# Performance work log

Hardware: AMD Instinct MI355X
Metric: run time of the kernel (lower is better)

Reference implementation:

```python
import jax, jax.numpy as jnp
import numpy as np

B, S, D, H, F = 2, 2048, 1024, 16, 4096
HD = D // H
NEG_INF = jnp.float32(-1e30)


def layer_norm(x, gamma, beta, eps=1e-6):
    mu = jnp.mean(x, axis=-1, keepdims=True)
    var = jnp.mean(jnp.square(x - mu), axis=-1, keepdims=True)
    return (x - mu) * jax.lax.rsqrt(var + eps) * gamma + beta


def setup_inputs() -> dict:
    key = jax.random.key(0)
    ks = jax.random.split(key, 8)
    d = np.sqrt(float(D))
    dx_up = np.sqrt(6.0 / (D + F))
    dx_dn = np.sqrt(6.0 / (F + D))
    return {
        "x_embeds": jax.random.normal(ks[0], (B, S, D), dtype=jnp.float32),
        "tokens": jax.random.randint(ks[1], (B, S), 0, 128, dtype=jnp.int32),
        "KQV": jax.random.uniform(ks[2], (D, 3 * D), jnp.float32, -1 / d, 1 / d),
        "WO": jax.random.uniform(ks[3], (D, D), jnp.float32, -1 / d, 1 / d),
        "W_up": jax.random.uniform(ks[4], (D, F), jnp.float32, -dx_up, dx_up),
        "b_up": jnp.zeros((F,), jnp.float32),
        "W_down": jax.random.uniform(ks[5], (F, D), jnp.float32, -dx_dn, dx_dn),
        "b_down": jnp.zeros((D,), jnp.float32),
        "ln1_g": jnp.ones((D,), jnp.float32),
        "ln1_b": jnp.zeros((D,), jnp.float32),
        "ln2_g": jnp.ones((D,), jnp.float32),
        "ln2_b": jnp.zeros((D,), jnp.float32),
        "start_token_id": 1,
    }


def reference(x_embeds, tokens, KQV, WO, W_up, b_up, W_down, b_down,
              ln1_g, ln1_b, ln2_g, ln2_b, start_token_id):
    b, s = x_embeds.shape[0], x_embeds.shape[1]
    # --- attention ---
    x_kqv = jnp.einsum("bsd,de->bse", x_embeds, KQV)          # [B,S,3D]
    x_kqv = x_kqv.reshape(b, s, H, 3, HD)
    k = x_kqv[:, :, :, 0, :]   # [B,S,H,HD]
    q = x_kqv[:, :, :, 1, :]
    v = x_kqv[:, :, :, 2, :]
    inner = jnp.einsum("bqhd,bkhd->bhqk", q, k)               # [B,H,S,S]
    # causal mask
    causal = jnp.tril(jnp.ones((s, s), dtype=bool))           # [S,S]
    # block-diagonal document mask from start tokens
    seg = jnp.cumsum((tokens == start_token_id).astype(jnp.int32), axis=1)  # [B,S]
    same_seg = seg[:, :, None] == seg[:, None, :]             # [B,S,S]
    mask = causal[None, None] & same_seg[:, None]             # [B,1->H,S,S]
    inner = jnp.where(mask, inner, NEG_INF)
    dk = jnp.sqrt(jnp.float32(HD))
    WA = jax.nn.softmax(inner / dk, axis=-1)
    head_outs = jnp.einsum("bhqk,bkhd->bqhd", WA, v)          # [B,S,H,HD]
    out = head_outs.reshape(b, s, D) @ WO
    out = layer_norm(out, ln1_g, ln1_b)
    x = out + x_embeds
    # --- ffnn ---
    h = jax.nn.relu(x @ W_up + b_up)
    out = h @ W_down + b_down
    out = layer_norm(out, ln2_g, ln2_b)
    return out + x
```

## Files before the change

### kernel.cpp

```cpp
#include <hip/hip_runtime.h>

typedef unsigned short u16;
typedef unsigned int u32;
typedef __bf16 bf16_t;
typedef bf16_t bf16x8 __attribute__((ext_vector_type(8)));
typedef u16 u16x8 __attribute__((ext_vector_type(8)));
typedef float f32x4 __attribute__((ext_vector_type(4)));

__device__ __forceinline__ float bf2f(u16 u) {
    union { float f; unsigned i; } c; c.i = ((unsigned)u) << 16; return c.f;
}
__device__ __forceinline__ u16 f2bf(float f) {
    return __builtin_bit_cast(u16, (bf16_t)f);
}
__device__ __forceinline__ f32x4 mfma16(bf16x8 a, bf16x8 b, f32x4 c) {
    return __builtin_amdgcn_mfma_f32_16x16x32_bf16(a, b, c, 0, 0, 0);
}
__device__ __forceinline__ void gld16(const u16* g, u16* l) {
    __builtin_amdgcn_global_load_lds(
        (const __attribute__((address_space(1))) void*)g,
        (__attribute__((address_space(3))) void*)l, 16, 0, 0);
}

__global__ __launch_bounds__(256)
void cvt_kernel(const float* __restrict__ in, u16* __restrict__ out)
{
    const int i = (blockIdx.x * 256 + threadIdx.x) * 8;
    float4 a = *reinterpret_cast<const float4*>(in + i);
    float4 b = *reinterpret_cast<const float4*>(in + i + 4);
    u16x8 o;
    o[0] = f2bf(a.x); o[1] = f2bf(a.y); o[2] = f2bf(a.z); o[3] = f2bf(a.w);
    o[4] = f2bf(b.x); o[5] = f2bf(b.y); o[6] = f2bf(b.z); o[7] = f2bf(b.w);
    *reinterpret_cast<u16x8*>(out + i) = o;
}

__global__ __launch_bounds__(256)
void cvt_t_kernel(const float* __restrict__ in, u16* __restrict__ out,
                  int K, int N)
{
    __shared__ float tile[32][33];
    const int kb = blockIdx.x * 32, nb = blockIdx.y * 32;
    const int r = threadIdx.x >> 3, c4 = threadIdx.x & 7;
    float4 v = *reinterpret_cast<const float4*>(&in[(size_t)(kb + r) * N + nb + c4 * 4]);
    tile[r][c4 * 4 + 0] = v.x; tile[r][c4 * 4 + 1] = v.y;
    tile[r][c4 * 4 + 2] = v.z; tile[r][c4 * 4 + 3] = v.w;
    __syncthreads();
    ushort4 o;
    o.x = f2bf(tile[c4 * 4 + 0][r]);
    o.y = f2bf(tile[c4 * 4 + 1][r]);
    o.z = f2bf(tile[c4 * 4 + 2][r]);
    o.w = f2bf(tile[c4 * 4 + 3][r]);
    *reinterpret_cast<ushort4*>(&out[(size_t)(nb + r) * K + kb + c4 * 4]) = o;
}

template<int NSPLIT, bool BIAS, bool RELU, bool QSCALE>
__global__ __launch_bounds__(512, 4)
void gemm8w_kernel(const u16* __restrict__ A, const u16* __restrict__ Bt,
                   const float* __restrict__ bias, u16* __restrict__ C,
                   int M, int N, int K)
{
    __shared__ u16 As[128][64];
    __shared__ u16 Bs[128][64];
    const int tid  = threadIdx.x;
    const int lane = tid & 63;
    const int wid  = tid >> 6;
    const int wm = wid >> 2, wn = wid & 3;
    const int bm = blockIdx.x, bn = blockIdx.y;
    const int kg = lane >> 4;
    const int lc = lane & 15;
    const int pk = kg ^ ((lc + (lc >> 2)) & 3);

    f32x4 acc[4][2];
    #pragma unroll
    for (int i = 0; i < 4; ++i)
        #pragma unroll
        for (int j = 0; j < 2; ++j)
            acc[i][j] = f32x4{0.f, 0.f, 0.f, 0.f};

    const int nk = (K >> 6) / NSPLIT;
    const int kbase = (NSPLIT > 1) ? blockIdx.z * nk : 0;

    for (int kt = 0; kt < nk; ++kt) {
        const int ktg = kbase + kt;
        __syncthreads();
        #pragma unroll
        for (int p = 0; p < 2; ++p) {
            int c = p * 512 + tid;
            int row  = c >> 3;
            int half = (c >> 2) & 1;
            int ko   = (((c & 3) ^ ((row + (row >> 2)) & 3)) << 3) + half * 32;
            gld16(A + (size_t)(bm * 128 + row) * K + ktg * 64 + ko,
                  &As[0][0] + c * 8);
            gld16(Bt + (size_t)(bn * 128 + row) * K + ktg * 64 + ko,
                  &Bs[0][0] + c * 8);
        }
        __syncthreads();

        bf16x8 af[4][2], bf[2][2];
        #pragma unroll
        for (int i = 0; i < 4; ++i)
            #pragma unroll
            for (int kk = 0; kk < 2; ++kk)
                af[i][kk] = *reinterpret_cast<const bf16x8*>(
                    &As[wm * 64 + i * 16 + lc][kk * 32 + pk * 8]);
        #pragma unroll
        for (int j = 0; j < 2; ++j)
            #pragma unroll
            for (int kk = 0; kk < 2; ++kk)
                bf[j][kk] = *reinterpret_cast<const bf16x8*>(
                    &Bs[wn * 32 + j * 16 + lc][kk * 32 + pk * 8]);
        #pragma unroll
        for (int j = 0; j < 2; ++j)
            #pragma unroll
            for (int i = 0; i < 4; ++i)
                #pragma unroll
                for (int kk = 0; kk < 2; ++kk)
                    acc[i][j] = mfma16(af[i][kk], bf[j][kk], acc[i][j]);
    }

    u16* Cp = C + (size_t)((NSPLIT > 1) ? blockIdx.z : 0) * M * N;
    const bool addb = BIAS && (NSPLIT == 1 || blockIdx.z == 0);
    #pragma unroll
    for (int i = 0; i < 4; ++i) {
        #pragma unroll
        for (int j = 0; j < 2; ++j) {
            int col = bn * 128 + wn * 32 + j * 16 + lc;
            float bv = addb ? bias[col] : 0.f;
            float qs = 1.0f;
            if (QSCALE) {
                u32 cm = (u32)col % 192u;
                if (cm >= 64u && cm < 128u) qs = 0.1803368875f;
            }
            #pragma unroll
            for (int r = 0; r < 4; ++r) {
                int row = bm * 128 + wm * 64 + i * 16 + kg * 4 + r;
                float v = acc[i][j][r] + bv;
                if (RELU) v = v > 0.f ? v : 0.f;
                if (QSCALE) v *= qs;
                Cp[(size_t)row * N + col] = f2bf(v);
            }
        }
    }
}

__global__ __launch_bounds__(256)
void qlo_kernel(const int* __restrict__ tokens, const int* __restrict__ start_id,
                int* __restrict__ qlo)
{
    constexpr int S = 2048;
    __shared__ int part[256];
    __shared__ int pref[256];
    const int b = blockIdx.x, tid = threadIdx.x;
    const int sid = start_id[0];
    const int base = b * S + tid * 8;
    int f[8]; int loc = -1;
    #pragma unroll
    for (int j = 0; j < 8; ++j) {
        f[j] = (tokens[base + j] == sid) ? 1 : 0;
        if (f[j]) loc = tid * 8 + j;
    }
    part[tid] = loc;
    __syncthreads();
    if (tid == 0) {
        int run = -1;
        for (int i = 0; i < 256; ++i) { pref[i] = run; run = max(run, part[i]); }
    }
    __syncthreads();
    int run = pref[tid];
    #pragma unroll
    for (int j = 0; j < 8; ++j) {
        if (f[j]) run = tid * 8 + j;
        qlo[base + j] = max(run, 0);
    }
}

#define MASKVAL -60000.0f
#define MINIT   -30000.0f
__global__ __launch_bounds__(256)
void attn_kernel(const u16* __restrict__ qkv, const int* __restrict__ qloA,
                 u16* __restrict__ attn_out)
{
    constexpr int S = 2048, DQ = 3072;
    __shared__ u16 Ks[64][72];
    __shared__ u16 Vt[64][72];
    __shared__ u16 Pt[4][16][72];
    __shared__ int wm4[4];

    const int tid = threadIdx.x;
    const int lane = tid & 63, w = tid >> 6;
    const int kg = lane >> 4, lc = lane & 15;
    const int qt = blockIdx.x, h = blockIdx.y, b = blockIdx.z;
    const size_t rowbase = (size_t)b * S;
    const int colK = h * 192, colQ = colK + 64, colV = colK + 128;
    const int qrow = qt * 64 + w * 16 + lc;

    bf16x8 qf0, qf1;
    {
        const u16* qp = &qkv[(rowbase + qrow) * DQ + colQ];
        qf0 = *reinterpret_cast<const bf16x8*>(qp + kg * 8);
        qf1 = *reinterpret_cast<const bf16x8*>(qp + 32 + kg * 8);
    }
    const int myqlo = qloA[rowbase + qrow];

    int vmin = myqlo;
    #pragma unroll
    for (int m = 1; m < 16; m <<= 1) vmin = min(vmin, __shfl_xor(vmin, m));
    if (lane == 0) wm4[w] = vmin;
    __syncthreads();
    const int kb0 = min(min(wm4[0], wm4[1]), min(wm4[2], wm4[3])) >> 6;

    float m_ = MINIT, l_ = 0.f;
    f32x4 o[4];
    #pragma unroll
    for (int d = 0; d < 4; ++d) o[d] = f32x4{0.f, 0.f, 0.f, 0.f};

    const int kr = tid >> 3, kc = tid & 7;
    const int rpv = tid >> 3, chv = tid & 7;
    uint4 gk0, gk1, gv0, gv1;

    auto issue = [&](int kb) {
        const size_t base = rowbase + (size_t)kb * 64;
        gk0 = *reinterpret_cast<const uint4*>(&qkv[(base + kr) * DQ + colK + kc * 8]);
        gk1 = *reinterpret_cast<const uint4*>(&qkv[(base + 32 + kr) * DQ + colK + kc * 8]);
        const u16* vp = &qkv[(base + rpv * 2) * DQ + colV + chv * 8];
        gv0 = *reinterpret_cast<const uint4*>(vp);
        gv1 = *reinterpret_cast<const uint4*>(vp + DQ);
    };
    auto write_lds = [&]() {
        *reinterpret_cast<uint4*>(&Ks[kr][kc * 8]) = gk0;
        *reinterpret_cast<uint4*>(&Ks[32 + kr][kc * 8]) = gk1;
        u16x8 va = __builtin_bit_cast(u16x8, gv0);
        u16x8 vb = __builtin_bit_cast(u16x8, gv1);
        const int kp = (rpv * 2) ^ (chv << 3);
        #pragma unroll
        for (int j = 0; j < 8; ++j)
            *reinterpret_cast<u32*>(&Vt[chv * 8 + j][kp]) =
                (u32)va[j] | ((u32)vb[j] << 16);
    };

    issue(kb0);
    for (int kb = kb0; kb <= qt; ++kb) {
        write_lds();
        __syncthreads();
        if (kb < qt) issue(kb + 1);

        f32x4 sT[4];
        #pragma unroll
        for (int ks = 0; ks < 4; ++ks) {
            bf16x8 kf0 = *reinterpret_cast<const bf16x8*>(&Ks[ks * 16 + lc][kg * 8]);
            bf16x8 kf1 = *reinterpret_cast<const bf16x8*>(&Ks[ks * 16 + lc][32 + kg * 8]);
            f32x4 s = f32x4{0.f, 0.f, 0.f, 0.f};
            s = mfma16(kf0, qf0, s);
            s = mfma16(kf1, qf1, s);
            sT[ks] = s;
        }
        const int lo = myqlo - kb * 64, hi = qrow - kb * 64;
        #pragma unroll
        for (int ks = 0; ks < 4; ++ks) {
            #pragma unroll
            for (int r = 0; r < 4; ++r) {
                int kk = ks * 16 + kg * 4 + r;
                bool ok = (kk >= lo) && (kk <= hi);
                sT[ks][r] = ok ? sT[ks][r] : MASKVAL;
            }
        }
        float tm = fmaxf(fmaxf(fmaxf(sT[0][0], sT[0][1]), fmaxf(sT[0][2], sT[0][3])),
                         fmaxf(fmaxf(sT[1][0], sT[1][1]), fmaxf(sT[1][2], sT[1][3])));
        tm = fmaxf(tm, fmaxf(fmaxf(fmaxf(sT[2][0], sT[2][1]), fmaxf(sT[2][2], sT[2][3])),
                             fmaxf(fmaxf(sT[3][0], sT[3][1]), fmaxf(sT[3][2], sT[3][3]))));
        tm = fmaxf(tm, __shfl_xor(tm, 16));
        tm = fmaxf(tm, __shfl_xor(tm, 32));
        float mn = fmaxf(m_, tm);
        float al = exp2f(m_ - mn);
        m_ = mn;
        float ps = 0.f;
        #pragma unroll
        for (int ks = 0; ks < 4; ++ks) {
            ushort4 pw;
            float p0 = exp2f(sT[ks][0] - m_); ps += p0; pw.x = f2bf(p0);
            float p1 = exp2f(sT[ks][1] - m_); ps += p1; pw.y = f2bf(p1);
            float p2 = exp2f(sT[ks][2] - m_); ps += p2; pw.z = f2bf(p2);
            float p3 = exp2f(sT[ks][3] - m_); ps += p3; pw.w = f2bf(p3);
            *reinterpret_cast<ushort4*>(&Pt[w][lc][ks * 16 + kg * 4]) = pw;
        }
        ps += __shfl_xor(ps, 16);
        ps += __shfl_xor(ps, 32);
        l_ = l_ * al + ps;
        float alr[4];
        #pragma unroll
        for (int r = 0; r < 4; ++r) alr[r] = __shfl(al, kg * 4 + r);
        #pragma unroll
        for (int d = 0; d < 4; ++d)
            #pragma unroll
            for (int r = 0; r < 4; ++r) o[d][r] *= alr[r];

        #pragma unroll
        for (int kf = 0; kf < 2; ++kf) {
            bf16x8 pf = *reinterpret_cast<const bf16x8*>(&Pt[w][lc][kf * 32 + kg * 8]);
            #pragma unroll
            for (int d = 0; d < 4; ++d) {
                int vrow = d * 16 + lc;
                int b3 = (kf * 4 + kg) ^ ((vrow >> 3) & 7);
                bf16x8 vf = *reinterpret_cast<const bf16x8*>(&Vt[vrow][b3 * 8]);
                o[d] = mfma16(pf, vf, o[d]);
            }
        }
        __syncthreads();
    }

    float lr[4];
    #pragma unroll
    for (int r = 0; r < 4; ++r) lr[r] = __shfl(l_, kg * 4 + r);
    #pragma unroll
    for (int d = 0; d < 4; ++d)
        #pragma unroll
        for (int r = 0; r < 4; ++r) {
            float v = o[d][r] / fmaxf(lr[r], 1e-20f);
            int qo = qt * 64 + w * 16 + kg * 4 + r;
            attn_out[(rowbase + qo) * 1024 + h * 64 + d * 16 + lc] = f2bf(v);
        }
}

template<int NSPL, bool WRITE_BF>
__global__ __launch_bounds__(256)
void ln_kernel(const u16* __restrict__ in, const float* __restrict__ gam,
               const float* __restrict__ bet, const float* res,
               float* out_f, u16* __restrict__ out_bf)
{
    const int row = blockIdx.x;
    const int tid = threadIdx.x;
    const int lane = tid & 63, w = tid >> 6;
    __shared__ float red1[4], red2[4];

    const size_t base = (size_t)row * 1024 + tid * 4;
    float x0 = 0.f, x1 = 0.f, x2 = 0.f, x3 = 0.f;
    #pragma unroll
    for (int sp = 0; sp < NSPL; ++sp) {
        ushort4 xv = *reinterpret_cast<const ushort4*>(in + (size_t)sp * 4194304 + base);
        x0 += bf2f(xv.x); x1 += bf2f(xv.y); x2 += bf2f(xv.z); x3 += bf2f(xv.w);
    }

    float s = x0 + x1 + x2 + x3;
    #pragma unroll
    for (int m = 1; m < 64; m <<= 1) s += __shfl_xor(s, m);
    if (lane == 0) red1[w] = s;
    __syncthreads();
    float mu = (red1[0] + red1[1] + red1[2] + red1[3]) * (1.0f / 1024.0f);

    float d0 = x0 - mu, d1 = x1 - mu, d2 = x2 - mu, d3 = x3 - mu;
    float q = d0 * d0 + d1 * d1 + d2 * d2 + d3 * d3;
    #pragma unroll
    for (int m = 1; m < 64; m <<= 1) q += __shfl_xor(q, m);
    if (lane == 0) red2[w] = q;
    __syncthreads();
    float var = (red2[0] + red2[1] + red2[2] + red2[3]) * (1.0f / 1024.0f);
    float rs = rsqrtf(var + 1e-6f);

    float dd[4] = {d0, d1, d2, d3};
    #pragma unroll
    for (int e = 0; e < 4; ++e) {
        int col = tid * 4 + e;
        size_t idx = (size_t)row * 1024 + col;
        float y = dd[e] * rs * gam[col] + bet[col];
        float ov = y + res[idx];
        out_f[idx] = ov;
        if constexpr (WRITE_BF) out_bf[idx] = f2bf(ov);
    }
}

extern "C" void kernel_launch(void* const* d_in, const int* in_sizes, int n_in,
                              void* d_out, int out_size, void* d_ws, size_t ws_size,
                              hipStream_t stream)
{
    const float* x_emb = (const float*)d_in[0];
    const int* tokens  = (const int*)d_in[1];
    const float* KQV   = (const float*)d_in[2];
    const float* WO    = (const float*)d_in[3];
    const float* W_up  = (const float*)d_in[4];
    const float* b_up  = (const float*)d_in[5];
    const float* W_dn  = (const float*)d_in[6];
    const float* b_dn  = (const float*)d_in[7];
    const float* g1    = (const float*)d_in[8];
    const float* be1   = (const float*)d_in[9];
    const float* g2    = (const float*)d_in[10];
    const float* be2   = (const float*)d_in[11];
    const int* start   = (const int*)d_in[12];

    const size_t MiB = 1048576;
    char* ws = (char*)d_ws;
    u16* XB     = (u16*)(ws + 0);
    u16* qkv    = (u16*)(ws + 8 * MiB);
    u16* attn_o = (u16*)(ws + 32 * MiB);
    u16* KBt    = (u16*)(ws + 40 * MiB);
    int* qloA   = (int*)(ws + 46 * MiB);
    u16* WOBt   = (u16*)(ws + 0);
    u16* cpart  = (u16*)(ws + 8 * MiB);
    u16* x_bf   = (u16*)(ws + 0);
    u16* WUBt   = (u16*)(ws + 40 * MiB);
    u16* hbuf   = (u16*)(ws + 8 * MiB);
    u16* WDBt   = (u16*)(ws + 0);
    u16* fpart  = (u16*)(ws + 40 * MiB);
    float* x_f  = (float*)d_out;
    float* outp = (float*)d_out;

    cvt_kernel<<<2048, 256, 0, stream>>>(x_emb, XB);
    cvt_t_kernel<<<dim3(32, 96), 256, 0, stream>>>(KQV, KBt, 1024, 3072);
    qlo_kernel<<<2, 256, 0, stream>>>(tokens, start, qloA);
    gemm8w_kernel<1, false, false, true><<<dim3(32, 24), 512, 0, stream>>>(XB, KBt, nullptr, qkv, 4096, 3072, 1024);
    cvt_t_kernel<<<dim3(32, 32), 256, 0, stream>>>(WO, WOBt, 1024, 1024);
    attn_kernel<<<dim3(32, 16, 2), 256, 0, stream>>>(qkv, qloA, attn_o);
    cvt_t_kernel<<<dim3(32, 128), 256, 0, stream>>>(W_up, WUBt, 1024, 4096);
    gemm8w_kernel<2, false, false, false><<<dim3(32, 8, 2), 512, 0, stream>>>(attn_o, WOBt, nullptr, cpart, 4096, 1024, 1024);
    ln_kernel<2, true><<<4096, 256, 0, stream>>>(cpart, g1, be1, x_emb, x_f, x_bf);
    gemm8w_kernel<1, true, true, false><<<dim3(32, 32), 512, 0, stream>>>(x_bf, WUBt, b_up, hbuf, 4096, 4096, 1024);
    cvt_t_kernel<<<dim3(128, 32), 256, 0, stream>>>(W_dn, WDBt, 4096, 1024);
    if (ws_size >= 72 * MiB) {
        gemm8w_kernel<4, true, false, false><<<dim3(32, 8, 4), 512, 0, stream>>>(hbuf, WDBt, b_dn, fpart, 4096, 1024, 4096);
        ln_kernel<4, false><<<4096, 256, 0, stream>>>(fpart, g2, be2, x_f, outp, nullptr);
    } else if (ws_size >= 56 * MiB) {
        gemm8w_kernel<2, true, false, false><<<dim3(32, 8, 2), 512, 0, stream>>>(hbuf, WDBt, b_dn, fpart, 4096, 1024, 4096);
        ln_kernel<2, false><<<4096, 256, 0, stream>>>(fpart, g2, be2, x_f, outp, nullptr);
    } else {
        gemm8w_kernel<1, true, false, false><<<dim3(32, 8), 512, 0, stream>>>(hbuf, WDBt, b_dn, fpart, 4096, 1024, 4096);
        ln_kernel<1, false><<<4096, 256, 0, stream>>>(fpart, g2, be2, x_f, outp, nullptr);
    }
}
```

Baseline: 224.4 us.

## Triple-buffer GEMM LDS tiles with async loads and one barrier per K-step

Reworks the bf16 GEMM main loop into a three-stage software pipeline. Each stage is a 32-wide K slice loaded straight into LDS two steps ahead, with explicit vmcnt waits and a single barrier per step in place of two. Wave priority is raised around the MFMA block, and the launch-bounds occupancy hint goes from 4 to 6. The aim is to hide global-load latency behind compute, at the cost of more barriers per unit of K and tighter register and occupancy limits.

```diff
diff --git a/kernel.cpp b/kernel.cpp
--- a/kernel.cpp
+++ b/kernel.cpp
@@ -21,6 +21,7 @@
         (const __attribute__((address_space(1))) void*)g,
         (__attribute__((address_space(3))) void*)l, 16, 0, 0);
 }
+#define SCHED_FENCE() __builtin_amdgcn_sched_barrier(0)
 
 __global__ __launch_bounds__(256)
 void cvt_kernel(const float* __restrict__ in, u16* __restrict__ out)
@@ -54,13 +55,13 @@
 }
 
 template<int NSPLIT, bool BIAS, bool RELU, bool QSCALE>
-__global__ __launch_bounds__(512, 4)
+__global__ __launch_bounds__(512, 6)
 void gemm8w_kernel(const u16* __restrict__ A, const u16* __restrict__ Bt,
                    const float* __restrict__ bias, u16* __restrict__ C,
                    int M, int N, int K)
 {
-    __shared__ u16 As[128][64];
-    __shared__ u16 Bs[128][64];
+    __shared__ u16 As[3][128][32];
+    __shared__ u16 Bs[3][128][32];
     const int tid  = threadIdx.x;
     const int lane = tid & 63;
     const int wid  = tid >> 6;
@@ -77,46 +78,52 @@
         for (int j = 0; j < 2; ++j)
             acc[i][j] = f32x4{0.f, 0.f, 0.f, 0.f};
 
-    const int nk = (K >> 6) / NSPLIT;
+    const int nk = (K >> 5) / NSPLIT;
     const int kbase = (NSPLIT > 1) ? blockIdx.z * nk : 0;
 
-    for (int kt = 0; kt < nk; ++kt) {
+    const int srow = tid >> 2;
+    const int sko  = ((tid & 3) ^ ((srow + (srow >> 2)) & 3)) * 8;
+
+    auto stage = [&](int t) {
+        const int kt = t < nk ? t : nk - 1;
+        const int buf = t % 3;
         const int ktg = kbase + kt;
-        __syncthreads();
-        #pragma unroll
-        for (int p = 0; p < 2; ++p) {
-            int c = p * 512 + tid;
-            int row  = c >> 3;
-            int half = (c >> 2) & 1;
-            int ko   = (((c & 3) ^ ((row + (row >> 2)) & 3)) << 3) + half * 32;
-            gld16(A + (size_t)(bm * 128 + row) * K + ktg * 64 + ko,
-                  &As[0][0] + c * 8);
-            gld16(Bt + (size_t)(bn * 128 + row) * K + ktg * 64 + ko,
-                  &Bs[0][0] + c * 8);
-        }
-        __syncthreads();
-
-        bf16x8 af[4][2], bf[2][2];
+        gld16(A + (size_t)(bm * 128 + srow) * K + ktg * 32 + sko,
+              &As[buf][0][0] + tid * 8);
+        gld16(Bt + (size_t)(bn * 128 + srow) * K + ktg * 32 + sko,
+              &Bs[buf][0][0] + tid * 8);
+    };
+
+    stage(0);
+    stage(1);
+    asm volatile("s_waitcnt vmcnt(2)" ::: "memory");
+    SCHED_FENCE();
+    __builtin_amdgcn_s_barrier();
+    SCHED_FENCE();
+
+    for (int t = 0; t < nk; ++t) {
+        const int cur = t % 3;
+        stage(t + 2);
+        bf16x8 af[4], bf[2];
         #pragma unroll
         for (int i = 0; i < 4; ++i)
-            #pragma unroll
-            for (int kk = 0; kk < 2; ++kk)
-                af[i][kk] = *reinterpret_cast<const bf16x8*>(
-                    &As[wm * 64 + i * 16 + lc][kk * 32 + pk * 8]);
+            af[i] = *reinterpret_cast<const bf16x8*>(&As[cur][wm * 64 + i * 16 + lc][pk * 8]);
         #pragma unroll
         for (int j = 0; j < 2; ++j)
-            #pragma unroll
-            for (int kk = 0; kk < 2; ++kk)
-                bf[j][kk] = *reinterpret_cast<const bf16x8*>(
-                    &Bs[wn * 32 + j * 16 + lc][kk * 32 + pk * 8]);
+            bf[j] = *reinterpret_cast<const bf16x8*>(&Bs[cur][wn * 32 + j * 16 + lc][pk * 8]);
+        __builtin_amdgcn_s_setprio(1);
         #pragma unroll
         for (int j = 0; j < 2; ++j)
             #pragma unroll
             for (int i = 0; i < 4; ++i)
-                #pragma unroll
-                for (int kk = 0; kk < 2; ++kk)
-                    acc[i][j] = mfma16(af[i][kk], bf[j][kk], acc[i][j]);
-    }
+                acc[i][j] = mfma16(af[i], bf[j], acc[i][j]);
+        __builtin_amdgcn_s_setprio(0);
+        asm volatile("s_waitcnt vmcnt(2)" ::: "memory");
+        SCHED_FENCE();
+        __builtin_amdgcn_s_barrier();
+        SCHED_FENCE();
+    }
+    asm volatile("s_waitcnt vmcnt(0)" ::: "memory");
 
     u16* Cp = C + (size_t)((NSPLIT > 1) ? blockIdx.z : 0) * M * N;
     const bool addb = BIAS && (NSPLIT == 1 || blockIdx.z == 0);
```

Result: slower. 243.0 us (+8.3%).
